# Optimization experiments

Measured on AMD Instinct MI355X. Metric: run time of the kernel, lower is better.

Reference implementation:

```python
import jax, jax.numpy as jnp
import numpy as np

EPS = 1e-6
B, S, H, I = 4, 2048, 2048, 8192  # batch, seq, hidden(embed), intermediate(mlp)
N_ACT = 2  # gated: ('gelu', 'linear')


def setup_inputs() -> dict:
    key = jax.random.key(0)
    k_x, k_k1, k_k2 = jax.random.split(key, 3)
    x = jax.random.normal(k_x, (B, S, H), dtype=jnp.float32)
    scale = jnp.ones((H,), dtype=jnp.float32)          # layernorm gamma (ones init)
    ln_bias = jnp.zeros((H,), dtype=jnp.float32)       # layernorm beta (zeros init)
    # kernel_1: (hidden, n_activations, intermediate); kernel_2: (intermediate, hidden)
    kernel_1 = jax.random.normal(k_k1, (H, N_ACT, I), dtype=jnp.float32) * 0.02
    kernel_2 = jax.random.normal(k_k2, (I, H), dtype=jnp.float32) * 0.02
    return {"x": x, "scale": scale, "ln_bias": ln_bias, "kernel_1": kernel_1, "kernel_2": kernel_2}


def reference(x, scale, ln_bias, kernel_1, kernel_2):
    # LayerNorm over last axis (zero_centered_gamma=False)
    mean = jnp.mean(x, axis=-1, keepdims=True)
    var = jnp.mean(jnp.square(x - mean), axis=-1, keepdims=True)
    ln = (x - mean) * jax.lax.rsqrt(var + EPS) * scale + ln_bias  # [B,S,H]
    # Dense 1: project to (n_activations, intermediate)
    y = jnp.einsum('bsh,hai->bsai', ln, kernel_1)  # [B,S,2,I]
    # Gated activation: gelu(y0) * linear(y1)  (flax nn.gelu default approximate=True)
    z = jax.nn.gelu(y[..., 0, :], approximate=True) * y[..., 1, :]  # [B,S,I]
    # Dense 2: project back to hidden
    out = jnp.einsum('bsi,ih->bsh', z, kernel_2)  # [B,S,H]
    return out
```

## Files before the change

### kernel.cpp

```cpp
#include <hip/hip_runtime.h>
#include <hip/hip_bf16.h>

#define DEVINL __device__ __forceinline__

typedef __attribute__((ext_vector_type(8))) __bf16 bf16x8;
typedef __attribute__((ext_vector_type(4))) float f32x4;
typedef __attribute__((ext_vector_type(4))) unsigned short us4;

DEVINL unsigned short f2bf(float f) {
  union { float f; unsigned int u; } c;
  c.f = f;
  unsigned int u = c.u;
  u += 0x7fffu + ((u >> 16) & 1u);
  return (unsigned short)(u >> 16);
}

DEVINL float gelu_tanh(float x) {
  float t = 1.5957691216057308f * x * __builtin_fmaf(0.044715f, x * x, 1.0f);
  return x / (1.0f + __expf(-t));
}

DEVINL void ld16(const void* g, void* l) {
  __builtin_amdgcn_global_load_lds(
      (const __attribute__((address_space(1))) void*)g,
      (__attribute__((address_space(3))) void*)l, 16, 0, 0);
}

__global__ __launch_bounds__(256) void transpose_cast_kernel(
    const float* __restrict__ in, unsigned short* __restrict__ out, int R, int C) {
  __shared__ float tile[32][33];
  const int t = threadIdx.x;
  const int r0 = blockIdx.x << 5, c0 = blockIdx.y << 5;
  const int tr = t >> 3, tc = (t & 7) << 2;
  const float4 v = *(const float4*)(in + (size_t)(r0 + tr) * C + c0 + tc);
  tile[tr][tc] = v.x; tile[tr][tc + 1] = v.y;
  tile[tr][tc + 2] = v.z; tile[tr][tc + 3] = v.w;
  __syncthreads();
  us4 o;
  o[0] = f2bf(tile[tc + 0][tr]);
  o[1] = f2bf(tile[tc + 1][tr]);
  o[2] = f2bf(tile[tc + 2][tr]);
  o[3] = f2bf(tile[tc + 3][tr]);
  *(us4*)(out + (size_t)(c0 + tr) * R + r0 + tc) = o;
}

__global__ __launch_bounds__(256) void ln_kernel(
    const float* __restrict__ x, const float* __restrict__ gamma,
    const float* __restrict__ beta, unsigned short* __restrict__ out) {
  constexpr int H = 2048;
  const int t = threadIdx.x;
  const size_t row = blockIdx.x;
  const float4* xr = (const float4*)(x + row * H);
  const float4 a = xr[t], b = xr[t + 256];
  float s  = a.x + a.y + a.z + a.w + b.x + b.y + b.z + b.w;
  float s2 = a.x*a.x + a.y*a.y + a.z*a.z + a.w*a.w
           + b.x*b.x + b.y*b.y + b.z*b.z + b.w*b.w;
#pragma unroll
  for (int o = 32; o > 0; o >>= 1) { s += __shfl_xor(s, o); s2 += __shfl_xor(s2, o); }
  __shared__ float red[8];
  const int wid = t >> 6, lane = t & 63;
  if (lane == 0) { red[wid] = s; red[4 + wid] = s2; }
  __syncthreads();
  s  = red[0] + red[1] + red[2] + red[3];
  s2 = red[4] + red[5] + red[6] + red[7];
  const float mean = s * (1.0f / H);
  const float rstd = rsqrtf(s2 * (1.0f / H) - mean * mean + 1e-6f);
  const float4 g0 = ((const float4*)gamma)[t], g1 = ((const float4*)gamma)[t + 256];
  const float4 c0 = ((const float4*)beta)[t],  c1 = ((const float4*)beta)[t + 256];
  us4 o0, o1;
  o0[0] = f2bf((a.x - mean) * rstd * g0.x + c0.x);
  o0[1] = f2bf((a.y - mean) * rstd * g0.y + c0.y);
  o0[2] = f2bf((a.z - mean) * rstd * g0.z + c0.z);
  o0[3] = f2bf((a.w - mean) * rstd * g0.w + c0.w);
  o1[0] = f2bf((b.x - mean) * rstd * g1.x + c1.x);
  o1[1] = f2bf((b.y - mean) * rstd * g1.y + c1.y);
  o1[2] = f2bf((b.z - mean) * rstd * g1.z + c1.z);
  o1[3] = f2bf((b.w - mean) * rstd * g1.w + c1.w);
  *(us4*)(out + row * H + (size_t)t * 4) = o0;
  *(us4*)(out + row * H + 1024 + (size_t)t * 4) = o1;
}

template<int KDIM, bool GATED>
__global__ __launch_bounds__(512, 2) void gemm8p(
    const unsigned short* __restrict__ Amat,
    const unsigned short* __restrict__ Bm0,
    const unsigned short* __restrict__ Bm1,
    void* __restrict__ outp, int mCount) {
  constexpr int NT = KDIM / 64;
  __shared__ char lds[131072];
  const int t = threadIdx.x, lane = t & 63, wid = t >> 6;
  const int wr = wid >> 2, wc = wid & 3;
  const int bid = (int)blockIdx.x;
  int mb, nb;
  if (GATED && mCount >= 8) {
    const int xcd = bid & 7, l = bid >> 3;
    const int g = l >> 5, l32 = l & 31;
    const int mchunks = mCount >> 3;
    const int quad = g / mchunks, mch = g % mchunks;
    mb = (mch << 3) | (l32 & 7);
    nb = (xcd << 3) | (quad << 2) | (l32 >> 3);
  } else {
    const int nwg = (int)gridDim.x, q = nwg >> 3;
    const int wg = (bid & 7) * q + (bid >> 3);
    mb = wg % mCount; nb = wg / mCount;
  }
  const size_t m0 = (size_t)mb << 8;
  const size_t nrow = (size_t)nb * (GATED ? 128 : 256);
  const unsigned short* aSrc  = Amat + m0 * KDIM;
  const unsigned short* b0Src = Bm0 + nrow * KDIM;
  const unsigned short* b1Src = Bm1 + nrow * KDIM;

  const int srow = (wid << 3) + (lane >> 3);
  const int sOff = srow * KDIM + (((lane & 7) ^ (srow & 7)) << 3);

  const int fr = lane & 15, l16 = lane >> 4;
  const int c0 = (l16 ^ (fr & 7)) << 4;
  const int c1 = ((4 | l16) ^ (fr & 7)) << 4;
  const int aRowOff = ((wr << 6) + fr) << 7;
  const int bRowOff = ((wc << 5) + fr) << 7;

  f32x4 acc[2][2][4][2] = {};

  auto stageU = [&](const unsigned short* src, int ldsOff, int k0) {
    const unsigned short* s = src + sOff + k0;
    ld16(s, lds + ldsOff + (wid << 10));
    ld16(s + (size_t)64 * KDIM, lds + ldsOff + 8192 + (wid << 10));
  };

#define RD_AM(ab_, m_)                                                        \
  af[0][m_] = *(const bf16x8*)((ab_) + aRowOff + (m_) * 2048 + c0);           \
  af[1][m_] = *(const bf16x8*)((ab_) + aRowOff + (m_) * 2048 + c1);
#define READ_A(ab_)                                                           \
  { RD_AM(ab_, 0) RD_AM(ab_, 1) RD_AM(ab_, 2) RD_AM(ab_, 3) }
#define READ_B(dst_, bb_)                                                     \
  _Pragma("unroll") for (int n = 0; n < 2; ++n) {                             \
    dst_[0][n] = *(const bf16x8*)((bb_) + bRowOff + n * 2048 + c0);           \
    dst_[1][n] = *(const bf16x8*)((bb_) + bRowOff + n * 2048 + c1);           \
  }
#define MFMA_G(mh_, g_, m_, bsrc_)                                            \
  _Pragma("unroll") for (int n = 0; n < 2; ++n) {                             \
    acc[mh_][g_][m_][n] = __builtin_amdgcn_mfma_f32_16x16x32_bf16(            \
        af[0][m_], bsrc_[0][n], acc[mh_][g_][m_][n], 0, 0, 0);                \
    acc[mh_][g_][m_][n] = __builtin_amdgcn_mfma_f32_16x16x32_bf16(            \
        af[1][m_], bsrc_[1][n], acc[mh_][g_][m_][n], 0, 0, 0);                \
  }
#define MFMA_CL(mh_, g_, bsrc_)                                               \
  { MFMA_G(mh_, g_, 0, bsrc_) MFMA_G(mh_, g_, 1, bsrc_)                       \
    MFMA_G(mh_, g_, 2, bsrc_) MFMA_G(mh_, g_, 3, bsrc_) }
#define LGKM(n_)                                                              \
  asm volatile("s_waitcnt lgkmcnt(" #n_ ")" ::: "memory");                    \
  __builtin_amdgcn_sched_barrier(0);
#define SCHED0 __builtin_amdgcn_sched_barrier(0)

  stageU(aSrc, 0, 0);
  stageU(b0Src, 32768, 0);
  stageU(aSrc + (size_t)128 * KDIM, 16384, 0);
  stageU(b1Src, 49152, 0);
  stageU(aSrc, 65536, NT > 1 ? 64 : 0);
  stageU(b0Src, 65536 + 32768, NT > 1 ? 64 : 0);
  asm volatile("s_waitcnt vmcnt(4)" ::: "memory");
  __builtin_amdgcn_s_barrier();

  bf16x8 af[2][4], b0r[2][2], b1r[2][2];
  READ_B(b1r, lds + 49152);  SCHED0;
  READ_A(lds);               SCHED0;
  READ_B(b0r, lds + 32768);  SCHED0;

  for (int tt = 0; tt < NT; ++tt) {
    const int c = tt & 1, cn = c ^ 1;
    const int t1 = (tt + 1 < NT) ? tt + 1 : NT - 1;
    const int t2 = (tt + 2 < NT) ? tt + 2 : NT - 1;
    const int k1b = t1 << 6, k2b = t2 << 6;
    const int cb = c << 16, cnb = cn << 16;
    const char* base = lds + cb;
    const char* nbase = lds + cnb;
    const char* hib = base + 16384;

    LGKM(0);
    stageU(aSrc + (size_t)128 * KDIM, cnb + 16384, k1b);
    stageU(b1Src, cnb + 49152, k1b);
    __builtin_amdgcn_s_setprio(1);
    MFMA_CL(0, 0, b0r);
    MFMA_G(0, 1, 0, b1r); RD_AM(hib, 0) SCHED0;
    MFMA_G(0, 1, 1, b1r); RD_AM(hib, 1) SCHED0;
    MFMA_G(0, 1, 2, b1r); RD_AM(hib, 2) SCHED0;
    MFMA_G(0, 1, 3, b1r); RD_AM(hib, 3) SCHED0;
    __builtin_amdgcn_s_setprio(0);
    LGKM(0);
    __builtin_amdgcn_s_barrier();
    stageU(aSrc, cb, k2b);
    stageU(b0Src, cb + 32768, k2b);
    asm volatile("s_waitcnt vmcnt(4)" ::: "memory");
    SCHED0;
    __builtin_amdgcn_s_barrier();

    __builtin_amdgcn_s_setprio(1);
    MFMA_CL(1, 1, b1r);
    READ_B(b1r, nbase + 49152); SCHED0;
    MFMA_G(1, 0, 0, b0r); RD_AM(nbase, 0) SCHED0;
    MFMA_G(1, 0, 1, b0r); RD_AM(nbase, 1) SCHED0;
    MFMA_G(1, 0, 2, b0r); RD_AM(nbase, 2) SCHED0;
    MFMA_G(1, 0, 3, b0r); RD_AM(nbase, 3) SCHED0;
    __builtin_amdgcn_s_setprio(0);
    READ_B(b0r, nbase + 32768); SCHED0;
  }
  asm volatile("s_waitcnt vmcnt(0) lgkmcnt(0)" ::: "memory");
#undef RD_AM
#undef READ_A
#undef READ_B
#undef MFMA_G
#undef MFMA_CL
#undef LGKM
#undef SCHED0

  const int fq = (lane >> 4) << 2;
  if constexpr (GATED) {
    unsigned short* Z = (unsigned short*)outp;
#pragma unroll
    for (int mh = 0; mh < 2; ++mh)
#pragma unroll
      for (int m = 0; m < 4; ++m)
#pragma unroll
        for (int n = 0; n < 2; ++n) {
          const size_t row = m0 + (mh << 7) + (wr << 6) + (m << 4) + fq;
          const size_t col = ((size_t)nb << 7) + (wc << 5) + (n << 4) + fr;
#pragma unroll
          for (int rr = 0; rr < 4; ++rr) {
            const float y0 = acc[mh][0][m][n][rr];
            const float y1 = acc[mh][1][m][n][rr];
            Z[(row + rr) * 8192 + col] = f2bf(gelu_tanh(y0) * y1);
          }
        }
  } else {
    float* O = (float*)outp;
#pragma unroll
    for (int mh = 0; mh < 2; ++mh)
#pragma unroll
      for (int g = 0; g < 2; ++g)
#pragma unroll
        for (int m = 0; m < 4; ++m)
#pragma unroll
          for (int n = 0; n < 2; ++n) {
            const size_t row = m0 + (mh << 7) + (wr << 6) + (m << 4) + fq;
            const size_t col = ((size_t)nb << 8) + (g << 7) + (wc << 5) + (n << 4) + fr;
#pragma unroll
            for (int rr = 0; rr < 4; ++rr)
              O[(row + rr) * 2048 + col] = acc[mh][g][m][n][rr];
          }
  }
}

extern "C" void kernel_launch(void* const* d_in, const int* in_sizes, int n_in,
                              void* d_out, int out_size, void* d_ws, size_t ws_size,
                              hipStream_t stream) {
  const float* x     = (const float*)d_in[0];
  const float* gamma = (const float*)d_in[1];
  const float* beta  = (const float*)d_in[2];
  const float* k1    = (const float*)d_in[3];
  const float* k2    = (const float*)d_in[4];
  float* out = (float*)d_out;

  const size_t H = 2048, I = 8192, M = 8192;
  unsigned short* k1T = (unsigned short*)d_ws;
  unsigned short* k2T = k1T + 2 * I * H;
  unsigned short* lnb = k2T + H * I;
  unsigned short* zb  = lnb + M * H;

  const size_t fixedB = (2 * I * H + H * I + M * H) * 2;
  int nc = 1;
  while (nc < 32 && fixedB + (M / nc) * I * 2 > ws_size) nc <<= 1;

  transpose_cast_kernel<<<dim3(H / 32, (2 * I) / 32), 256, 0, stream>>>(
      k1, k1T, (int)H, (int)(2 * I));
  transpose_cast_kernel<<<dim3(I / 32, H / 32), 256, 0, stream>>>(
      k2, k2T, (int)I, (int)H);
  ln_kernel<<<dim3((unsigned)M), 256, 0, stream>>>(x, gamma, beta, lnb);

  const size_t Mc = M / nc;
  const int mC = (int)(Mc / 256);
  for (int c = 0; c < nc; ++c) {
    gemm8p<2048, true><<<dim3((unsigned)(mC * 64)), 512, 0, stream>>>(
        lnb + c * Mc * H, k1T, k1T + (size_t)8192 * 2048, zb, mC);
    gemm8p<8192, false><<<dim3((unsigned)(mC * 8)), 512, 0, stream>>>(
        zb, k2T, k2T + (size_t)128 * 8192, out + c * Mc * H, mC);
  }
}
```

Measured before the change: 771.0 us.

## Switch GEMM inner loop from 16x16x32 to 32x32x16 bf16 MFMA tiles

Replaces the 16x16x32 MFMA fragments with 32x32x16 MFMA instructions. Each wave now holds 2x2x2 accumulators of 16 floats and reads A and B fragments in four k-chunks per 64-wide k tile. This cuts the number of MFMA issues and LDS fragment reads per tile, at the cost of reordering the interleave of LDS reads and MFMAs within the pipelined loop. The epilogue is rewritten to match the 32x32 output layout. Register pressure and the changed placement of the wait points may reduce the overlap between LDS reads and compute.

```diff
diff --git a/kernel.cpp b/kernel.cpp
--- a/kernel.cpp
+++ b/kernel.cpp
@@ -4,7 +4,7 @@
 #define DEVINL __device__ __forceinline__
 
 typedef __attribute__((ext_vector_type(8))) __bf16 bf16x8;
-typedef __attribute__((ext_vector_type(4))) float f32x4;
+typedef __attribute__((ext_vector_type(16))) float f32x16;
 typedef __attribute__((ext_vector_type(4))) unsigned short us4;
 
 DEVINL unsigned short f2bf(float f) {
@@ -81,7 +81,7 @@
 }
 
 template<int KDIM, bool GATED>
-__global__ __launch_bounds__(512, 2) void gemm8p(
+__global__ __launch_bounds__(512, 2) void gemm32(
     const unsigned short* __restrict__ Amat,
     const unsigned short* __restrict__ Bm0,
     const unsigned short* __restrict__ Bm1,
@@ -113,13 +113,16 @@
   const int srow = (wid << 3) + (lane >> 3);
   const int sOff = srow * KDIM + (((lane & 7) ^ (srow & 7)) << 3);
 
-  const int fr = lane & 15, l16 = lane >> 4;
-  const int c0 = (l16 ^ (fr & 7)) << 4;
-  const int c1 = ((4 | l16) ^ (fr & 7)) << 4;
-  const int aRowOff = ((wr << 6) + fr) << 7;
-  const int bRowOff = ((wc << 5) + fr) << 7;
-
-  f32x4 acc[2][2][4][2] = {};
+  const int l31 = lane & 31, l5 = lane >> 5;
+  int chunkOff[4];
+#pragma unroll
+  for (int ks = 0; ks < 4; ++ks)
+    chunkOff[ks] = (((ks << 1) + l5) ^ (l31 & 7)) << 4;
+  const int rowA0 = ((wr << 6) + l31) << 7;
+  const int rowA1 = ((wr << 6) + 32 + l31) << 7;
+  const int rowB  = ((wc << 5) + l31) << 7;
+
+  f32x16 acc[2][2][2] = {};
 
   auto stageU = [&](const unsigned short* src, int ldsOff, int k0) {
     const unsigned short* s = src + sOff + k0;
@@ -127,26 +130,28 @@
     ld16(s + (size_t)64 * KDIM, lds + ldsOff + 8192 + (wid << 10));
   };
 
-#define RD_AM(ab_, m_)                                                        \
-  af[0][m_] = *(const bf16x8*)((ab_) + aRowOff + (m_) * 2048 + c0);           \
-  af[1][m_] = *(const bf16x8*)((ab_) + aRowOff + (m_) * 2048 + c1);
-#define READ_A(ab_)                                                           \
-  { RD_AM(ab_, 0) RD_AM(ab_, 1) RD_AM(ab_, 2) RD_AM(ab_, 3) }
+#define RD_AF_MM(ab_, mm_)                                                    \
+  _Pragma("unroll") for (int ks = 0; ks < 4; ++ks)                            \
+    af[ks][mm_] = *(const bf16x8*)((ab_) + ((mm_) ? rowA1 : rowA0) + chunkOff[ks]);
+#define READ_AF(ab_) { RD_AF_MM(ab_, 0) RD_AF_MM(ab_, 1) }
 #define READ_B(dst_, bb_)                                                     \
-  _Pragma("unroll") for (int n = 0; n < 2; ++n) {                             \
-    dst_[0][n] = *(const bf16x8*)((bb_) + bRowOff + n * 2048 + c0);           \
-    dst_[1][n] = *(const bf16x8*)((bb_) + bRowOff + n * 2048 + c1);           \
-  }
-#define MFMA_G(mh_, g_, m_, bsrc_)                                            \
-  _Pragma("unroll") for (int n = 0; n < 2; ++n) {                             \
-    acc[mh_][g_][m_][n] = __builtin_amdgcn_mfma_f32_16x16x32_bf16(            \
-        af[0][m_], bsrc_[0][n], acc[mh_][g_][m_][n], 0, 0, 0);                \
-    acc[mh_][g_][m_][n] = __builtin_amdgcn_mfma_f32_16x16x32_bf16(            \
-        af[1][m_], bsrc_[1][n], acc[mh_][g_][m_][n], 0, 0, 0);                \
-  }
-#define MFMA_CL(mh_, g_, bsrc_)                                               \
-  { MFMA_G(mh_, g_, 0, bsrc_) MFMA_G(mh_, g_, 1, bsrc_)                       \
-    MFMA_G(mh_, g_, 2, bsrc_) MFMA_G(mh_, g_, 3, bsrc_) }
+  _Pragma("unroll") for (int ks = 0; ks < 4; ++ks)                            \
+    dst_[ks] = *(const bf16x8*)((bb_) + rowB + chunkOff[ks]);
+#define MFMA_SUPER(mh_)                                                       \
+  _Pragma("unroll") for (int ks = 0; ks < 4; ++ks)                            \
+    _Pragma("unroll") for (int mm = 0; mm < 2; ++mm) {                        \
+      acc[mh_][0][mm] = __builtin_amdgcn_mfma_f32_32x32x16_bf16(              \
+          af[ks][mm], b0r[ks], acc[mh_][0][mm], 0, 0, 0);                     \
+      acc[mh_][1][mm] = __builtin_amdgcn_mfma_f32_32x32x16_bf16(              \
+          af[ks][mm], b1r[ks], acc[mh_][1][mm], 0, 0, 0);                     \
+    }
+#define MFMA_MM(mh_, mm_)                                                     \
+  _Pragma("unroll") for (int ks = 0; ks < 4; ++ks) {                          \
+    acc[mh_][0][mm_] = __builtin_amdgcn_mfma_f32_32x32x16_bf16(               \
+        af[ks][mm_], b0r[ks], acc[mh_][0][mm_], 0, 0, 0);                     \
+    acc[mh_][1][mm_] = __builtin_amdgcn_mfma_f32_32x32x16_bf16(               \
+        af[ks][mm_], b1r[ks], acc[mh_][1][mm_], 0, 0, 0);                     \
+  }
 #define LGKM(n_)                                                              \
   asm volatile("s_waitcnt lgkmcnt(" #n_ ")" ::: "memory");                    \
   __builtin_amdgcn_sched_barrier(0);
@@ -161,10 +166,10 @@
   asm volatile("s_waitcnt vmcnt(4)" ::: "memory");
   __builtin_amdgcn_s_barrier();
 
-  bf16x8 af[2][4], b0r[2][2], b1r[2][2];
+  bf16x8 af[4][2], b0r[4], b1r[4];
+  READ_AF(lds);              SCHED0;
+  READ_B(b0r, lds + 32768);  SCHED0;
   READ_B(b1r, lds + 49152);  SCHED0;
-  READ_A(lds);               SCHED0;
-  READ_B(b0r, lds + 32768);  SCHED0;
 
   for (int tt = 0; tt < NT; ++tt) {
     const int c = tt & 1, cn = c ^ 1;
@@ -174,20 +179,18 @@
     const int cb = c << 16, cnb = cn << 16;
     const char* base = lds + cb;
     const char* nbase = lds + cnb;
-    const char* hib = base + 16384;
-
-    LGKM(0);
+
     stageU(aSrc + (size_t)128 * KDIM, cnb + 16384, k1b);
     stageU(b1Src, cnb + 49152, k1b);
+    LGKM(0);
     __builtin_amdgcn_s_setprio(1);
-    MFMA_CL(0, 0, b0r);
-    MFMA_G(0, 1, 0, b1r); RD_AM(hib, 0) SCHED0;
-    MFMA_G(0, 1, 1, b1r); RD_AM(hib, 1) SCHED0;
-    MFMA_G(0, 1, 2, b1r); RD_AM(hib, 2) SCHED0;
-    MFMA_G(0, 1, 3, b1r); RD_AM(hib, 3) SCHED0;
+    MFMA_SUPER(0);
     __builtin_amdgcn_s_setprio(0);
+    SCHED0;
+    READ_AF(base + 16384);
     LGKM(0);
     __builtin_amdgcn_s_barrier();
+
     stageU(aSrc, cb, k2b);
     stageU(b0Src, cb + 32768, k2b);
     asm volatile("s_waitcnt vmcnt(4)" ::: "memory");
@@ -195,58 +198,55 @@
     __builtin_amdgcn_s_barrier();
 
     __builtin_amdgcn_s_setprio(1);
-    MFMA_CL(1, 1, b1r);
-    READ_B(b1r, nbase + 49152); SCHED0;
-    MFMA_G(1, 0, 0, b0r); RD_AM(nbase, 0) SCHED0;
-    MFMA_G(1, 0, 1, b0r); RD_AM(nbase, 1) SCHED0;
-    MFMA_G(1, 0, 2, b0r); RD_AM(nbase, 2) SCHED0;
-    MFMA_G(1, 0, 3, b0r); RD_AM(nbase, 3) SCHED0;
+    MFMA_MM(1, 0);
+    RD_AF_MM(nbase, 0) SCHED0;
+    MFMA_MM(1, 1);
+    RD_AF_MM(nbase, 1) SCHED0;
     __builtin_amdgcn_s_setprio(0);
     READ_B(b0r, nbase + 32768); SCHED0;
+    READ_B(b1r, nbase + 49152); SCHED0;
   }
   asm volatile("s_waitcnt vmcnt(0) lgkmcnt(0)" ::: "memory");
-#undef RD_AM
-#undef READ_A
+#undef RD_AF_MM
+#undef READ_AF
 #undef READ_B
-#undef MFMA_G
-#undef MFMA_CL
+#undef MFMA_SUPER
+#undef MFMA_MM
 #undef LGKM
 #undef SCHED0
 
-  const int fq = (lane >> 4) << 2;
   if constexpr (GATED) {
     unsigned short* Z = (unsigned short*)outp;
 #pragma unroll
     for (int mh = 0; mh < 2; ++mh)
 #pragma unroll
-      for (int m = 0; m < 4; ++m)
-#pragma unroll
-        for (int n = 0; n < 2; ++n) {
-          const size_t row = m0 + (mh << 7) + (wr << 6) + (m << 4) + fq;
-          const size_t col = ((size_t)nb << 7) + (wc << 5) + (n << 4) + fr;
-#pragma unroll
-          for (int rr = 0; rr < 4; ++rr) {
-            const float y0 = acc[mh][0][m][n][rr];
-            const float y1 = acc[mh][1][m][n][rr];
-            Z[(row + rr) * 8192 + col] = f2bf(gelu_tanh(y0) * y1);
+      for (int mm = 0; mm < 2; ++mm) {
+        const size_t rb = m0 + (mh << 7) + (wr << 6) + (mm << 5) + (l5 << 2);
+        const size_t col = ((size_t)nb << 7) + (wc << 5) + l31;
+#pragma unroll
+        for (int r = 0; r < 16; ++r) {
+          const size_t row = rb + (r & 3) + ((r >> 2) << 3);
+          const float y0 = acc[mh][0][mm][r];
+          const float y1 = acc[mh][1][mm][r];
+          Z[row * 8192 + col] = f2bf(gelu_tanh(y0) * y1);
+        }
+      }
+  } else {
+    float* O = (float*)outp;
+#pragma unroll
+    for (int mh = 0; mh < 2; ++mh)
+#pragma unroll
+      for (int g = 0; g < 2; ++g)
+#pragma unroll
+        for (int mm = 0; mm < 2; ++mm) {
+          const size_t rb = m0 + (mh << 7) + (wr << 6) + (mm << 5) + (l5 << 2);
+          const size_t col = ((size_t)nb << 8) + (g << 7) + (wc << 5) + l31;
+#pragma unroll
+          for (int r = 0; r < 16; ++r) {
+            const size_t row = rb + (r & 3) + ((r >> 2) << 3);
+            O[row * 2048 + col] = acc[mh][g][mm][r];
           }
         }
-  } else {
-    float* O = (float*)outp;
-#pragma unroll
-    for (int mh = 0; mh < 2; ++mh)
-#pragma unroll
-      for (int g = 0; g < 2; ++g)
-#pragma unroll
-        for (int m = 0; m < 4; ++m)
-#pragma unroll
-          for (int n = 0; n < 2; ++n) {
-            const size_t row = m0 + (mh << 7) + (wr << 6) + (m << 4) + fq;
-            const size_t col = ((size_t)nb << 8) + (g << 7) + (wc << 5) + (n << 4) + fr;
-#pragma unroll
-            for (int rr = 0; rr < 4; ++rr)
-              O[(row + rr) * 2048 + col] = acc[mh][g][m][n][rr];
-          }
   }
 }
 
@@ -279,9 +279,9 @@
   const size_t Mc = M / nc;
   const int mC = (int)(Mc / 256);
   for (int c = 0; c < nc; ++c) {
-    gemm8p<2048, true><<<dim3((unsigned)(mC * 64)), 512, 0, stream>>>(
+    gemm32<2048, true><<<dim3((unsigned)(mC * 64)), 512, 0, stream>>>(
         lnb + c * Mc * H, k1T, k1T + (size_t)8192 * 2048, zb, mC);
-    gemm8p<8192, false><<<dim3((unsigned)(mC * 8)), 512, 0, stream>>>(
+    gemm32<8192, false><<<dim3((unsigned)(mC * 8)), 512, 0, stream>>>(
         zb, k2T, k2T + (size_t)128 * 8192, out + c * Mc * H, mC);
   }
 }
```

Measured after the change: 845.2 us. 9.6% more time.
